# Kernel optimization log

Measured on AMD Instinct MI355X. Metric: run time of the kernel, lower is better.

Reference implementation:

```python
import jax, jax.numpy as jnp
import numpy as np

B, T, N, F_IN = 4, 16, 1000, 8
E = 8000
HID = 64
HEADS = 4
L = 5


def setup_inputs() -> dict:
    key = jax.random.key(0)
    ks = jax.random.split(key, 16)
    s = 0.1
    return {
        "x_seq": jax.random.normal(ks[0], (B, T, N, F_IN), dtype=jnp.float32),
        "edge_index": jax.random.randint(ks[1], (2, E), 0, N, dtype=jnp.int32),
        "edge_weight": jax.random.uniform(ks[2], (E,), dtype=jnp.float32),
        # input projection
        "W_in": jax.random.normal(ks[3], (F_IN, HID)) * s,
        "b_in": jnp.zeros((HID,), jnp.float32),
        # 5 stacked GATConv layers (heads=4, concat=False -> per-head dim = HID, mean over heads)
        "Wg": jax.random.normal(ks[4], (L, HID, HEADS * HID)) * s,
        "a_src": jax.random.normal(ks[5], (L, HEADS, HID)) * s,
        "a_dst": jax.random.normal(ks[6], (L, HEADS, HID)) * s,
        "bg": jnp.zeros((L, HID), jnp.float32),
        # GRU (input = N*HID flattened node features, torch gate order r,z,n)
        "W_ih": jax.random.normal(ks[7], (3 * HID, N * HID)) * 0.02,
        "W_hh": jax.random.normal(ks[8], (3 * HID, HID)) * s,
        "b_ih": jnp.zeros((3 * HID,), jnp.float32),
        "b_hh": jnp.zeros((3 * HID,), jnp.float32),
        # head: Linear(hidden_dim, num_nodes*pred_window) so out.view(B, N) works
        "W_fc": jax.random.normal(ks[9], (HID, N)) * s,
        "b_fc": jnp.zeros((N,), jnp.float32),
    }


def reference(x_seq, edge_index, edge_weight, W_in, b_in, Wg, a_src, a_dst, bg,
              W_ih, W_hh, b_ih, b_hh, W_fc, b_fc):
    Bb, Tt, Nn, Fin = x_seq.shape
    hid = W_in.shape[1]
    heads = a_src.shape[1]
    # PyG GATConv adds self-loops by default
    self_loops = jnp.arange(Nn, dtype=edge_index.dtype)
    src = jnp.concatenate([edge_index[0], self_loops])
    dst = jnp.concatenate([edge_index[1], self_loops])

    # input_fc over all (batch*seq*node) rows
    x = (x_seq.reshape(-1, Fin) @ W_in + b_in).reshape(Bb * Tt, Nn, hid)

    def gat_one(x_g, W, asrc, adst, b):
        h = (x_g @ W).reshape(Nn, heads, hid)            # [N,H,C]
        ls = (h * asrc).sum(-1)                          # [N,H] src attention terms
        ld = (h * adst).sum(-1)                          # [N,H] dst attention terms
        e = jax.nn.leaky_relu(ls[src] + ld[dst], 0.2)    # [E',H]
        m = jax.ops.segment_max(e, dst, num_segments=Nn)
        ex = jnp.exp(e - m[dst])
        den = jax.ops.segment_sum(ex, dst, num_segments=Nn)
        alpha = ex / (den[dst] + 1e-16)                  # softmax over incoming edges
        msg = alpha[:, :, None] * h[src]                 # [E',H,C]
        agg = jax.ops.segment_sum(msg, dst, num_segments=Nn)
        return agg.mean(axis=1) + b                      # concat=False -> mean heads

    for l in range(Wg.shape[0]):
        x = jax.nn.elu(jax.vmap(
            lambda xg, W=Wg[l], a1=a_src[l], a2=a_dst[l], b=bg[l]: gat_one(xg, W, a1, a2, b)
        )(x))

    # GRU over time, input = flattened node features per timestep
    seq = x.reshape(Bb, Tt, Nn * hid).transpose(1, 0, 2)  # [T,B,N*HID]

    def step(h, x_t):
        gi = x_t @ W_ih.T + b_ih
        gh = h @ W_hh.T + b_hh
        ir, iz, inn = jnp.split(gi, 3, axis=-1)
        hr, hz, hn = jnp.split(gh, 3, axis=-1)
        r = jax.nn.sigmoid(ir + hr)
        z = jax.nn.sigmoid(iz + hz)
        n = jnp.tanh(inn + r * hn)
        return (1.0 - z) * n + z * h, None

    h0 = jnp.zeros((Bb, hid), x_seq.dtype)
    hT, _ = jax.lax.scan(step, h0, seq)                  # last GRU output == final h
    return hT @ W_fc + b_fc                              # [B, N]
```

## Files before the change

### kernel.cpp

```cpp
#include <hip/hip_runtime.h>
#include <math.h>

#define NB 4
#define TT 16
#define NNODE 1000
#define FIN 8
#define EE 8000
#define EP 9000
#define EPAD 16384
#define HID 64
#define HEADS 4
#define NL 5
#define GG (NB*TT)
#define ROWS (GG*NNODE)
#define HCOL (HEADS*HID)
#define KGI (NNODE*HID)
#define GOUT 192
#define GIK 128
#define KSPLIT (KGI/GIK)
#define GOSZ (GG*GOUT)
#define WPSZ (8*4*64*8)

typedef unsigned short u16;
typedef __attribute__((ext_vector_type(8))) short short8;
typedef __attribute__((ext_vector_type(4))) float f32x4;

__device__ inline u16 f2bf(float f) {
    unsigned int u = __float_as_uint(f);
    unsigned int r = u + 0x7FFFu + ((u >> 16) & 1u);
    return (u16)(r >> 16);
}
__device__ inline float bf2f(u16 h) {
    return __uint_as_float(((unsigned int)h) << 16);
}

__global__ void k_build_edges(const int* __restrict__ eidx, int* __restrict__ src_e,
                              int* __restrict__ dst_e, int* __restrict__ deg, int* __restrict__ fill) {
    int i = blockIdx.x * blockDim.x + threadIdx.x;
    if (i < EP) {
        int s, d;
        if (i < EE) { s = eidx[i]; d = eidx[EE + i]; }
        else { s = i - EE; d = i - EE; }
        src_e[i] = s; dst_e[i] = d;
    }
    if (i < NNODE) { deg[i] = 0; fill[i] = 0; }
}

__global__ void k_csr_count(const int* __restrict__ dst_e, int* __restrict__ deg) {
    int i = blockIdx.x * blockDim.x + threadIdx.x;
    if (i < EP) atomicAdd(&deg[dst_e[i]], 1);
}

__global__ __launch_bounds__(256) void k_csr_scan(const int* __restrict__ deg, int* __restrict__ rowptr_p) {
    __shared__ int s[1024];
    int tid = threadIdx.x;
    for (int i = tid; i < 1024; i += 256) s[i] = (i < NNODE) ? ((deg[i] + 7) & ~7) : 0;
    __syncthreads();
    for (int off = 1; off < 1024; off <<= 1) {
        int t[4];
        #pragma unroll
        for (int q = 0; q < 4; q++) { int i = tid + 256 * q; t[q] = (i >= off) ? s[i - off] : 0; }
        __syncthreads();
        #pragma unroll
        for (int q = 0; q < 4; q++) { int i = tid + 256 * q; s[i] += t[q]; }
        __syncthreads();
    }
    for (int i = tid; i < NNODE; i += 256) rowptr_p[i + 1] = s[i];
    if (tid == 0) rowptr_p[0] = 0;
}

__global__ void k_csr_fill(const int* __restrict__ src_e, const int* __restrict__ dst_e,
                           const int* __restrict__ rowptr_p, int* __restrict__ fill,
                           int* __restrict__ csr_src) {
    int i = blockIdx.x * blockDim.x + threadIdx.x;
    if (i < EP) {
        int d = dst_e[i];
        int pos = atomicAdd(&fill[d], 1);
        csr_src[rowptr_p[d] + pos] = src_e[i];
    }
}

__global__ void k_pad_fill(const int* __restrict__ rowptr_p, const int* __restrict__ deg,
                           int* __restrict__ csr_src) {
    int n = blockIdx.x * blockDim.x + threadIdx.x;
    if (n >= NNODE) return;
    int rs = rowptr_p[n], re = rowptr_p[n + 1];
    for (int j = rs + deg[n]; j < re; j++) csr_src[j] = n;
}

__global__ void k_wa(const float* __restrict__ Wg, const float* __restrict__ a_src,
                     const float* __restrict__ a_dst, float* __restrict__ wa, float* __restrict__ wd) {
    int t = blockIdx.x * 256 + threadIdx.x;
    if (t >= 2 * NL * HID * HEADS) return;
    int kind = t >= NL * HID * HEADS;
    int u = t - kind * NL * HID * HEADS;
    int l = u >> 8;
    int rem = u & 255;
    int j = rem >> 2, hd = rem & 3;
    const float* a = (kind ? a_dst : a_src) + (size_t)l * HCOL + hd * HID;
    const float* Wl = Wg + (size_t)l * HID * HCOL + (size_t)j * HCOL + hd * HID;
    float acc = 0.f;
    #pragma unroll 8
    for (int c = 0; c < HID; c++) acc += Wl[c] * a[c];
    float* out = kind ? wd : wa;
    out[(size_t)l * HCOL + j * 4 + hd] = acc;
}

__global__ void k_wpack(const float* __restrict__ Wg, u16* __restrict__ wph, u16* __restrict__ wpl) {
    int t = blockIdx.x * 256 + threadIdx.x;
    if (t >= NL * WPSZ) return;
    int j    = t & 7;
    int lane = (t >> 3) & 63;
    int ct   = (t >> 9) & 3;
    int ks   = (t >> 11) & 7;
    int l    = t >> 14;
    int k = ks * 32 + (lane >> 4) * 8 + j;
    int c = ct * 16 + (lane & 15);
    float v = Wg[(size_t)l * HID * HCOL + (size_t)(k & 63) * HCOL + (k >> 6) * 64 + c];
    u16 h = f2bf(v);
    wph[t] = h;
    wpl[t] = f2bf(v - bf2f(h));
}

__global__ void k_input_fc(const float* __restrict__ xseq, const float4* __restrict__ Win4,
                           const float4* __restrict__ b_in4, const float4* __restrict__ wa04,
                           const float4* __restrict__ wd04, float4* __restrict__ x0,
                           float4* __restrict__ ls4, float4* __restrict__ ld4) {
    int idx = blockIdx.x * 256 + threadIdx.x;
    int r = idx >> 4, c4 = idx & 15;
    float4 acc = b_in4[c4];
    #pragma unroll
    for (int k = 0; k < FIN; k++) {
        float xv = xseq[r * FIN + k];
        float4 w = Win4[k * 16 + c4];
        acc.x += xv * w.x; acc.y += xv * w.y; acc.z += xv * w.z; acc.w += xv * w.w;
    }
    x0[idx] = acc;
    float xr[4] = {acc.x, acc.y, acc.z, acc.w};
    float4 pls = make_float4(0.f, 0.f, 0.f, 0.f);
    float4 pld = make_float4(0.f, 0.f, 0.f, 0.f);
    #pragma unroll
    for (int jj = 0; jj < 4; jj++) {
        float4 wa_j = wa04[c4 * 4 + jj];
        float4 wd_j = wd04[c4 * 4 + jj];
        pls.x += xr[jj] * wa_j.x; pls.y += xr[jj] * wa_j.y;
        pls.z += xr[jj] * wa_j.z; pls.w += xr[jj] * wa_j.w;
        pld.x += xr[jj] * wd_j.x; pld.y += xr[jj] * wd_j.y;
        pld.z += xr[jj] * wd_j.z; pld.w += xr[jj] * wd_j.w;
    }
    #pragma unroll
    for (int o = 1; o < 16; o <<= 1) {
        pls.x += __shfl_xor(pls.x, o, 64); pls.y += __shfl_xor(pls.y, o, 64);
        pls.z += __shfl_xor(pls.z, o, 64); pls.w += __shfl_xor(pls.w, o, 64);
        pld.x += __shfl_xor(pld.x, o, 64); pld.y += __shfl_xor(pld.y, o, 64);
        pld.z += __shfl_xor(pld.w, o, 64); pld.w += __shfl_xor(pld.w, o, 64);
    }
    if (c4 == 0) {
        ls4[r] = pls;
        ld4[r] = pld;
    }
}

__global__ __launch_bounds__(256) void k_aggx(const float4* __restrict__ x4, const float4* __restrict__ ls4,
                                              const float4* __restrict__ ld4, const int* __restrict__ rowptr_p,
                                              const int* __restrict__ csr_src, const int* __restrict__ deg,
                                              u16* __restrict__ yh, u16* __restrict__ yl) {
    __shared__ float s_e[4][4][4 * 68];
    __shared__ int   s_src[4][4][64];
    __shared__ float s_den[4][4][4];
    int b = blockIdx.x;
    int xcd = b & 7, s = b >> 3;
    int tid = threadIdx.x;
    int wid = tid >> 6, lane = tid & 63;
    int w = s * 4 + wid;
    int g = xcd + 8 * (w / 250);
    int n0 = (w % 250) * 4;
    int nsub = lane >> 4;
    int j0 = lane & 15;
    int n_s = n0 + nsub;
    int rs = rowptr_p[n_s];
    int dgp = rowptr_p[n_s + 1] - rs;
    int dg = deg[n_s];
    int dg16 = (dgp + 15) & ~15;
    if (dg16 > 64) dg16 = 64;
    if (dgp > 64) dgp = 64;
    float4 ldv = ld4[(size_t)g * NNODE + n_s];
    const float4* lsg = ls4 + (size_t)g * NNODE;

    float4 mx = make_float4(-1e30f, -1e30f, -1e30f, -1e30f);
    for (int base = 0; base < dg16; base += 16) {
        int j = base + j0;
        int sv = n_s;
        if (j < dgp) sv = csr_src[rs + j];
        s_src[wid][nsub][j] = sv;
        float4 lo = make_float4(-1e30f, -1e30f, -1e30f, -1e30f);
        if (j < dg) {
            float4 t = lsg[sv];
            t.x += ldv.x; t.y += ldv.y; t.z += ldv.z; t.w += ldv.w;
            t.x = fmaxf(t.x, 0.2f * t.x); t.y = fmaxf(t.y, 0.2f * t.y);
            t.z = fmaxf(t.z, 0.2f * t.z); t.w = fmaxf(t.w, 0.2f * t.w);
            lo = t;
            mx.x = fmaxf(mx.x, lo.x); mx.y = fmaxf(mx.y, lo.y);
            mx.z = fmaxf(mx.z, lo.z); mx.w = fmaxf(mx.w, lo.w);
        }
        s_e[wid][nsub][0 * 68 + j] = lo.x;
        s_e[wid][nsub][1 * 68 + j] = lo.y;
        s_e[wid][nsub][2 * 68 + j] = lo.z;
        s_e[wid][nsub][3 * 68 + j] = lo.w;
    }
    #pragma unroll
    for (int o = 1; o < 16; o <<= 1) {
        mx.x = fmaxf(mx.x, __shfl_xor(mx.x, o, 64));
        mx.y = fmaxf(mx.y, __shfl_xor(mx.y, o, 64));
        mx.z = fmaxf(mx.z, __shfl_xor(mx.z, o, 64));
        mx.w = fmaxf(mx.w, __shfl_xor(mx.w, o, 64));
    }
    float4 den = make_float4(0.f, 0.f, 0.f, 0.f);
    for (int base = 0; base < dg16; base += 16) {
        int j = base + j0;
        float4 e = make_float4(0.f, 0.f, 0.f, 0.f);
        if (j < dg) {
            e.x = expf(s_e[wid][nsub][0 * 68 + j] - mx.x);
            e.y = expf(s_e[wid][nsub][1 * 68 + j] - mx.y);
            e.z = expf(s_e[wid][nsub][2 * 68 + j] - mx.z);
            e.w = expf(s_e[wid][nsub][3 * 68 + j] - mx.w);
        }
        den.x += e.x; den.y += e.y; den.z += e.z; den.w += e.w;
        s_e[wid][nsub][0 * 68 + j] = e.x;
        s_e[wid][nsub][1 * 68 + j] = e.y;
        s_e[wid][nsub][2 * 68 + j] = e.z;
        s_e[wid][nsub][3 * 68 + j] = e.w;
    }
    #pragma unroll
    for (int o = 1; o < 16; o <<= 1) {
        den.x += __shfl_xor(den.x, o, 64);
        den.y += __shfl_xor(den.y, o, 64);
        den.z += __shfl_xor(den.z, o, 64);
        den.w += __shfl_xor(den.w, o, 64);
    }
    if (j0 == 0) {
        s_den[wid][nsub][0] = den.x;
        s_den[wid][nsub][1] = den.y;
        s_den[wid][nsub][2] = den.z;
        s_den[wid][nsub][3] = den.w;
    }

    int head = lane >> 4, c4 = lane & 15;
    const float4* xg = x4 + (size_t)g * NNODE * 16 + c4;
    float4 acc[4];
    #pragma unroll
    for (int nn = 0; nn < 4; nn++) acc[nn] = make_float4(0.f, 0.f, 0.f, 0.f);
    #pragma unroll
    for (int nn = 0; nn < 4; nn++) {
        int dgc = __shfl(dgp, nn * 16, 64);
        const float* ep = &s_e[wid][nn][head * 68];
        const int* sp = &s_src[wid][nn][0];
        for (int q = 0; q < dgc; q += 8) {
            int sj[8]; float av[8];
            #pragma unroll
            for (int u = 0; u < 8; u++) {
                sj[u] = sp[q + u];
                av[u] = ep[q + u];
            }
            float4 xv[8];
            #pragma unroll
            for (int u = 0; u < 8; u++) xv[u] = xg[(size_t)sj[u] * 16];
            #pragma unroll
            for (int u = 0; u < 8; u++) {
                acc[nn].x += av[u] * xv[u].x;
                acc[nn].y += av[u] * xv[u].y;
                acc[nn].z += av[u] * xv[u].z;
                acc[nn].w += av[u] * xv[u].w;
            }
        }
    }
    #pragma unroll
    for (int nn = 0; nn < 4; nn++) {
        float inv = 1.f / (s_den[wid][nn][head] + 1e-16f);
        float4 a = acc[nn];
        a.x *= inv; a.y *= inv; a.z *= inv; a.w *= inv;
        size_t r64 = ((size_t)g * NNODE + n0 + nn) * 64 + lane;
        ushort4 hv, lv;
        hv.x = f2bf(a.x); lv.x = f2bf(a.x - bf2f(hv.x));
        hv.y = f2bf(a.y); lv.y = f2bf(a.y - bf2f(hv.y));
        hv.z = f2bf(a.z); lv.z = f2bf(a.z - bf2f(hv.z));
        hv.w = f2bf(a.w); lv.w = f2bf(a.w - bf2f(hv.w));
        reinterpret_cast<ushort4*>(yh)[r64] = hv;
        reinterpret_cast<ushort4*>(yl)[r64] = lv;
    }
}

__global__ __launch_bounds__(256) void k_ygemm_mfma(const u16* __restrict__ yh, const u16* __restrict__ yl,
                                                    const u16* __restrict__ wph, const u16* __restrict__ wpl,
                                                    const float* __restrict__ bg, float* __restrict__ xout,
                                                    const float4* __restrict__ wa4, const float4* __restrict__ wd4,
                                                    float4* __restrict__ ls4, float4* __restrict__ ld4) {
    int tid = threadIdx.x;
    int wv = tid >> 6, lane = tid & 63;
    int r0w = blockIdx.x * 64 + wv * 16;
    int arow = lane & 15, kg = lane >> 4;

    f32x4 acc0 = {0.f, 0.f, 0.f, 0.f};
    f32x4 acc1 = {0.f, 0.f, 0.f, 0.f};
    f32x4 acc2 = {0.f, 0.f, 0.f, 0.f};
    f32x4 acc3 = {0.f, 0.f, 0.f, 0.f};

    const short8* ah8 = reinterpret_cast<const short8*>(yh + (size_t)(r0w + arow) * 256 + kg * 8);
    const short8* al8 = reinterpret_cast<const short8*>(yl + (size_t)(r0w + arow) * 256 + kg * 8);
    const short8* bh8 = reinterpret_cast<const short8*>(wph) + lane;
    const short8* bl8 = reinterpret_cast<const short8*>(wpl) + lane;

    #pragma unroll
    for (int ks = 0; ks < 8; ks++) {
        short8 ah = ah8[ks * 4];
        short8 al = al8[ks * 4];
        #pragma unroll
        for (int ct = 0; ct < 4; ct++) {
            short8 bh = bh8[(size_t)(ks * 4 + ct) * 64];
            short8 bl = bl8[(size_t)(ks * 4 + ct) * 64];
            f32x4* ac = (ct == 0) ? &acc0 : (ct == 1) ? &acc1 : (ct == 2) ? &acc2 : &acc3;
            *ac = __builtin_amdgcn_mfma_f32_16x16x32_bf16(ah, bh, *ac, 0, 0, 0);
            *ac = __builtin_amdgcn_mfma_f32_16x16x32_bf16(ah, bl, *ac, 0, 0, 0);
            *ac = __builtin_amdgcn_mfma_f32_16x16x32_bf16(al, bh, *ac, 0, 0, 0);
        }
    }

    float ev[4][4];
    #pragma unroll
    for (int ct = 0; ct < 4; ct++) {
        int c = ct * 16 + arow;
        float bc = bg[c];
        f32x4 a = (ct == 0) ? acc0 : (ct == 1) ? acc1 : (ct == 2) ? acc2 : acc3;
        #pragma unroll
        for (int r = 0; r < 4; r++) {
            float v = a[r] * 0.25f + bc;
            float e = v > 0.f ? v : expm1f(v);
            ev[ct][r] = e;
            xout[(size_t)(r0w + kg * 4 + r) * HID + c] = e;
        }
    }
    if (wa4) {
        #pragma unroll
        for (int r = 0; r < 4; r++) {
            float4 pls = make_float4(0.f, 0.f, 0.f, 0.f);
            float4 pld = make_float4(0.f, 0.f, 0.f, 0.f);
            #pragma unroll
            for (int ct = 0; ct < 4; ct++) {
                int c = ct * 16 + arow;
                float e = ev[ct][r];
                float4 wa_c = wa4[c];
                float4 wd_c = wd4[c];
                pls.x += e * wa_c.x; pls.y += e * wa_c.y;
                pls.z += e * wa_c.z; pls.w += e * wa_c.w;
                pld.x += e * wd_c.x; pld.y += e * wd_c.y;
                pld.z += e * wd_c.z; pld.w += e * wd_c.w;
            }
            #pragma unroll
            for (int o = 1; o < 16; o <<= 1) {
                pls.x += __shfl_xor(pls.x, o, 64); pls.y += __shfl_xor(pls.y, o, 64);
                pls.z += __shfl_xor(pls.z, o, 64); pls.w += __shfl_xor(pls.w, o, 64);
                pld.x += __shfl_xor(pld.x, o, 64); pld.y += __shfl_xor(pld.y, o, 64);
                pld.z += __shfl_xor(pld.z, o, 64); pld.w += __shfl_xor(pld.w, o, 64);
            }
            if (arow == 0) {
                int row = r0w + kg * 4 + r;
                ls4[row] = pls;
                ld4[row] = pld;
            }
        }
    }
}

__global__ __launch_bounds__(256) void k_gi_gemm(const float* __restrict__ x, const float* __restrict__ W_ih,
                                                 float* __restrict__ gip) {
    __shared__ float xs[32 * 68];
    __shared__ float ws[32 * 196];
    int k0 = blockIdx.x * GIK;
    int tid = threadIdx.x;
    int lane = tid & 63;
    int wv = tid >> 6;
    int tx = tid & 15, ty = tid >> 4;
    float4 accs[4][3];
    #pragma unroll
    for (int i = 0; i < 4; i++)
        #pragma unroll
        for (int j = 0; j < 3; j++) accs[i][j] = make_float4(0.f, 0.f, 0.f, 0.f);

    for (int kt = 0; kt < GIK / 32; kt++) {
        int kb = k0 + kt * 32;
        #pragma unroll
        for (int it = 0; it < 2; it++) {
            int kq = wv + 4 * it;
            float4 v = *reinterpret_cast<const float4*>(&x[(size_t)lane * KGI + kb + kq * 4]);
            int k = kq * 4;
            xs[(k + 0) * 68 + lane] = v.x;
            xs[(k + 1) * 68 + lane] = v.y;
            xs[(k + 2) * 68 + lane] = v.z;
            xs[(k + 3) * 68 + lane] = v.w;
        }
        #pragma unroll
        for (int cg = 0; cg < 3; cg++) {
            #pragma unroll
            for (int it = 0; it < 2; it++) {
                int kq = wv + 4 * it;
                int c = cg * 64 + lane;
                float4 v = *reinterpret_cast<const float4*>(&W_ih[(size_t)c * KGI + kb + kq * 4]);
                int k = kq * 4;
                ws[(k + 0) * 196 + c] = v.x;
                ws[(k + 1) * 196 + c] = v.y;
                ws[(k + 2) * 196 + c] = v.z;
                ws[(k + 3) * 196 + c] = v.w;
            }
        }
        __syncthreads();
        for (int kk = 0; kk < 32; kk++) {
            float4 xv = *reinterpret_cast<const float4*>(&xs[kk * 68 + ty * 4]);
            float4 w0 = *reinterpret_cast<const float4*>(&ws[kk * 196 + tx * 4]);
            float4 w1 = *reinterpret_cast<const float4*>(&ws[kk * 196 + 64 + tx * 4]);
            float4 w2 = *reinterpret_cast<const float4*>(&ws[kk * 196 + 128 + tx * 4]);
            #pragma unroll
            for (int i = 0; i < 4; i++) {
                float xi = (i == 0) ? xv.x : (i == 1) ? xv.y : (i == 2) ? xv.z : xv.w;
                accs[i][0].x += xi * w0.x; accs[i][0].y += xi * w0.y; accs[i][0].z += xi * w0.z; accs[i][0].w += xi * w0.w;
                accs[i][1].x += xi * w1.x; accs[i][1].y += xi * w1.y; accs[i][1].z += xi * w1.z; accs[i][1].w += xi * w1.w;
                accs[i][2].x += xi * w2.x; accs[i][2].y += xi * w2.y; accs[i][2].z += xi * w2.z; accs[i][2].w += xi * w2.w;
            }
        }
        __syncthreads();
    }
    float* out = gip + (size_t)blockIdx.x * GOSZ;
    #pragma unroll
    for (int i = 0; i < 4; i++)
        #pragma unroll
        for (int j = 0; j < 3; j++)
            *reinterpret_cast<float4*>(&out[(ty * 4 + i) * GOUT + j * 64 + tx * 4]) = accs[i][j];
}

__global__ void k_gi_reduce1(const float* __restrict__ gip, float* __restrict__ gip2) {
    int idx = blockIdx.x * 256 + threadIdx.x;
    const float* p = gip + (size_t)blockIdx.y * 50 * GOSZ + idx;
    float a = 0.f;
    #pragma unroll 5
    for (int s = 0; s < 50; s++) a += p[(size_t)s * GOSZ];
    gip2[blockIdx.y * GOSZ + idx] = a;
}

__global__ void k_gi_reduce2(const float* __restrict__ gip2, const float* __restrict__ b_ih,
                             float* __restrict__ gi) {
    int idx = blockIdx.x * 256 + threadIdx.x;
    float a = b_ih[idx % GOUT];
    #pragma unroll
    for (int y = 0; y < 10; y++) a += gip2[(size_t)y * GOSZ + idx];
    gi[idx] = a;
}

__global__ __launch_bounds__(192) void k_gru(const float* __restrict__ gi, const float* __restrict__ W_hh,
                                             const float* __restrict__ b_hh, float* __restrict__ hT) {
    __shared__ float hs[64];
    __shared__ float gh[192];
    int j = threadIdx.x;
    int b = blockIdx.x;
    float wrow[64];
    #pragma unroll
    for (int q = 0; q < 16; q++) {
        float4 v = *reinterpret_cast<const float4*>(&W_hh[(size_t)j * 64 + q * 4]);
        wrow[q * 4 + 0] = v.x; wrow[q * 4 + 1] = v.y;
        wrow[q * 4 + 2] = v.z; wrow[q * 4 + 3] = v.w;
    }
    float bj = b_hh[j];
    if (j < 64) hs[j] = 0.f;
    __syncthreads();
    for (int t = 0; t < TT; t++) {
        float a0 = 0.f, a1 = 0.f, a2 = 0.f, a3 = 0.f;
        #pragma unroll
        for (int q = 0; q < 16; q++) {
            float4 h4 = *reinterpret_cast<const float4*>(&hs[q * 4]);
            a0 += h4.x * wrow[q * 4 + 0];
            a1 += h4.y * wrow[q * 4 + 1];
            a2 += h4.z * wrow[q * 4 + 2];
            a3 += h4.w * wrow[q * 4 + 3];
        }
        gh[j] = bj + ((a0 + a1) + (a2 + a3));
        __syncthreads();
        if (j < 64) {
            int row = (b * TT + t) * GOUT;
            float ir = gi[row + j], iz = gi[row + 64 + j], in_ = gi[row + 128 + j];
            float r = 1.f / (1.f + expf(-(ir + gh[j])));
            float z = 1.f / (1.f + expf(-(iz + gh[64 + j])));
            float nv = tanhf(in_ + r * gh[128 + j]);
            hs[j] = (1.f - z) * nv + z * hs[j];
        }
        __syncthreads();
    }
    if (j < 64) hT[b * 64 + j] = hs[j];
}

__global__ void k_final(const float* __restrict__ hT, const float* __restrict__ W_fc,
                        const float* __restrict__ b_fc, float* __restrict__ out) {
    int idx = blockIdx.x * 256 + threadIdx.x;
    if (idx >= NB * NNODE) return;
    int b = idx / NNODE, n = idx % NNODE;
    float acc = b_fc[n];
    #pragma unroll
    for (int c = 0; c < HID; c++) acc += hT[b * HID + c] * W_fc[c * NNODE + n];
    out[idx] = acc;
}

extern "C" void kernel_launch(void* const* d_in, const int* in_sizes, int n_in,
                              void* d_out, int out_size, void* d_ws, size_t ws_size,
                              hipStream_t stream) {
    const float* x_seq  = (const float*)d_in[0];
    const int*   eidx   = (const int*)  d_in[1];
    const float* W_in   = (const float*)d_in[3];
    const float* b_in   = (const float*)d_in[4];
    const float* Wg     = (const float*)d_in[5];
    const float* a_src  = (const float*)d_in[6];
    const float* a_dst  = (const float*)d_in[7];
    const float* bg     = (const float*)d_in[8];
    const float* W_ih   = (const float*)d_in[9];
    const float* W_hh   = (const float*)d_in[10];
    const float* b_ih   = (const float*)d_in[11];
    const float* b_hh   = (const float*)d_in[12];
    const float* W_fc   = (const float*)d_in[13];
    const float* b_fc   = (const float*)d_in[14];
    float* out = (float*)d_out;

    float* wsf = (float*)d_ws;
    size_t off = 0;
    float* x0     = wsf + off; off += (size_t)ROWS * HID;
    float* ybuf   = wsf + off; off += (size_t)ROWS * HCOL;
    float* lsb    = wsf + off; off += (size_t)ROWS * HEADS;
    float* ldb    = wsf + off; off += (size_t)ROWS * HEADS;
    float* wab    = wsf + off; off += NL * HCOL;
    float* wdb    = wsf + off; off += NL * HCOL;
    float* gib    = wsf + off; off += GOSZ;
    float* hTb    = wsf + off; off += 256;
    u16* wphb     = (u16*)(wsf + off); off += NL * WPSZ / 2;
    u16* wplb     = (u16*)(wsf + off); off += NL * WPSZ / 2;
    int* ib = (int*)(wsf + off);
    int* src_e    = ib;          ib += EP;
    int* dst_e    = ib;          ib += EP;
    int* rowptr_p = ib;          ib += NNODE + 1;
    int* csr_src  = ib;          ib += EPAD;
    int* deg      = ib;          ib += NNODE;
    int* fill     = ib;          ib += NNODE;

    u16* yh = (u16*)ybuf;
    u16* yl = yh + (size_t)ROWS * HCOL;

    float* gip  = ybuf;
    float* gip2 = ybuf + (size_t)KSPLIT * GOSZ;

    k_build_edges<<<(EP + 255) / 256, 256, 0, stream>>>(eidx, src_e, dst_e, deg, fill);
    k_csr_count<<<(EP + 255) / 256, 256, 0, stream>>>(dst_e, deg);
    k_csr_scan<<<1, 256, 0, stream>>>(deg, rowptr_p);
    k_csr_fill<<<(EP + 255) / 256, 256, 0, stream>>>(src_e, dst_e, rowptr_p, fill, csr_src);
    k_pad_fill<<<(NNODE + 255) / 256, 256, 0, stream>>>(rowptr_p, deg, csr_src);

    k_wa<<<10, 256, 0, stream>>>(Wg, a_src, a_dst, wab, wdb);
    k_wpack<<<(NL * WPSZ + 255) / 256, 256, 0, stream>>>(Wg, wphb, wplb);

    k_input_fc<<<ROWS * 16 / 256, 256, 0, stream>>>(
        x_seq, (const float4*)W_in, (const float4*)b_in,
        (const float4*)wab, (const float4*)wdb, (float4*)x0, (float4*)lsb, (float4*)ldb);

    for (int l = 0; l < NL; l++) {
        k_aggx<<<ROWS / 16, 256, 0, stream>>>(
            (const float4*)x0, (const float4*)lsb, (const float4*)ldb, rowptr_p, csr_src, deg,
            yh, yl);
        const float4* wa_next = (l + 1 < NL) ? (const float4*)(wab + (size_t)(l + 1) * HCOL) : nullptr;
        const float4* wd_next = (l + 1 < NL) ? (const float4*)(wdb + (size_t)(l + 1) * HCOL) : nullptr;
        k_ygemm_mfma<<<ROWS / 64, 256, 0, stream>>>(
            yh, yl, wphb + (size_t)l * WPSZ, wplb + (size_t)l * WPSZ,
            bg + (size_t)l * HID, x0,
            wa_next, wd_next, (float4*)lsb, (float4*)ldb);
    }

    k_gi_gemm<<<KSPLIT, 256, 0, stream>>>(x0, W_ih, gip);
    k_gi_reduce1<<<dim3(GOSZ / 256, 10), 256, 0, stream>>>(gip, gip2);
    k_gi_reduce2<<<GOSZ / 256, 256, 0, stream>>>(gip2, b_ih, gib);
    k_gru<<<4, 192, 0, stream>>>(gib, W_hh, b_hh, hTb);
    k_final<<<(NB * NNODE + 255) / 256, 256, 0, stream>>>(hTb, W_fc, b_fc, out);
}
```

Before: 493.0 us.

## Restructure GAT aggregation so each lane-group handles one node across all heads

```diff
diff --git a/kernel.cpp b/kernel.cpp
--- a/kernel.cpp
+++ b/kernel.cpp
@@ -33,6 +33,15 @@
 __device__ inline float bf2f(u16 h) {
     return __uint_as_float(((unsigned int)h) << 16);
 }
+__device__ inline ushort4 bfhi4(float4 a) {
+    ushort4 r; r.x = f2bf(a.x); r.y = f2bf(a.y); r.z = f2bf(a.z); r.w = f2bf(a.w); return r;
+}
+__device__ inline ushort4 bflo4(float4 a, ushort4 h) {
+    ushort4 r;
+    r.x = f2bf(a.x - bf2f(h.x)); r.y = f2bf(a.y - bf2f(h.y));
+    r.z = f2bf(a.z - bf2f(h.z)); r.w = f2bf(a.w - bf2f(h.w));
+    return r;
+}
 
 __global__ void k_build_edges(const int* __restrict__ eidx, int* __restrict__ src_e,
                               int* __restrict__ dst_e, int* __restrict__ deg, int* __restrict__ fill) {
@@ -153,7 +162,7 @@
         pls.x += __shfl_xor(pls.x, o, 64); pls.y += __shfl_xor(pls.y, o, 64);
         pls.z += __shfl_xor(pls.z, o, 64); pls.w += __shfl_xor(pls.w, o, 64);
         pld.x += __shfl_xor(pld.x, o, 64); pld.y += __shfl_xor(pld.y, o, 64);
-        pld.z += __shfl_xor(pld.w, o, 64); pld.w += __shfl_xor(pld.w, o, 64);
+        pld.z += __shfl_xor(pld.z, o, 64); pld.w += __shfl_xor(pld.w, o, 64);
     }
     if (c4 == 0) {
         ls4[r] = pls;
@@ -165,7 +174,7 @@
                                               const float4* __restrict__ ld4, const int* __restrict__ rowptr_p,
                                               const int* __restrict__ csr_src, const int* __restrict__ deg,
                                               u16* __restrict__ yh, u16* __restrict__ yl) {
-    __shared__ float s_e[4][4][4 * 68];
+    __shared__ float s_e[4][4][264];
     __shared__ int   s_src[4][4][64];
     __shared__ float s_den[4][4][4];
     int b = blockIdx.x;
@@ -203,10 +212,7 @@
             mx.x = fmaxf(mx.x, lo.x); mx.y = fmaxf(mx.y, lo.y);
             mx.z = fmaxf(mx.z, lo.z); mx.w = fmaxf(mx.w, lo.w);
         }
-        s_e[wid][nsub][0 * 68 + j] = lo.x;
-        s_e[wid][nsub][1 * 68 + j] = lo.y;
-        s_e[wid][nsub][2 * 68 + j] = lo.z;
-        s_e[wid][nsub][3 * 68 + j] = lo.w;
+        *reinterpret_cast<float4*>(&s_e[wid][nsub][j * 4]) = lo;
     }
     #pragma unroll
     for (int o = 1; o < 16; o <<= 1) {
@@ -220,16 +226,14 @@
         int j = base + j0;
         float4 e = make_float4(0.f, 0.f, 0.f, 0.f);
         if (j < dg) {
-            e.x = expf(s_e[wid][nsub][0 * 68 + j] - mx.x);
-            e.y = expf(s_e[wid][nsub][1 * 68 + j] - mx.y);
-            e.z = expf(s_e[wid][nsub][2 * 68 + j] - mx.z);
-            e.w = expf(s_e[wid][nsub][3 * 68 + j] - mx.w);
+            float4 lo = *reinterpret_cast<const float4*>(&s_e[wid][nsub][j * 4]);
+            e.x = expf(lo.x - mx.x);
+            e.y = expf(lo.y - mx.y);
+            e.z = expf(lo.z - mx.z);
+            e.w = expf(lo.w - mx.w);
         }
         den.x += e.x; den.y += e.y; den.z += e.z; den.w += e.w;
-        s_e[wid][nsub][0 * 68 + j] = e.x;
-        s_e[wid][nsub][1 * 68 + j] = e.y;
-        s_e[wid][nsub][2 * 68 + j] = e.z;
-        s_e[wid][nsub][3 * 68 + j] = e.w;
+        *reinterpret_cast<float4*>(&s_e[wid][nsub][j * 4]) = e;
     }
     #pragma unroll
     for (int o = 1; o < 16; o <<= 1) {
@@ -239,55 +243,51 @@
         den.w += __shfl_xor(den.w, o, 64);
     }
     if (j0 == 0) {
-        s_den[wid][nsub][0] = den.x;
-        s_den[wid][nsub][1] = den.y;
-        s_den[wid][nsub][2] = den.z;
-        s_den[wid][nsub][3] = den.w;
-    }
-
-    int head = lane >> 4, c4 = lane & 15;
+        *reinterpret_cast<float4*>(&s_den[wid][nsub][0]) = den;
+    }
+
+    int c4 = lane & 15;
     const float4* xg = x4 + (size_t)g * NNODE * 16 + c4;
-    float4 acc[4];
-    #pragma unroll
-    for (int nn = 0; nn < 4; nn++) acc[nn] = make_float4(0.f, 0.f, 0.f, 0.f);
-    #pragma unroll
-    for (int nn = 0; nn < 4; nn++) {
-        int dgc = __shfl(dgp, nn * 16, 64);
-        const float* ep = &s_e[wid][nn][head * 68];
-        const int* sp = &s_src[wid][nn][0];
-        for (int q = 0; q < dgc; q += 8) {
-            int sj[8]; float av[8];
-            #pragma unroll
-            for (int u = 0; u < 8; u++) {
-                sj[u] = sp[q + u];
-                av[u] = ep[q + u];
-            }
-            float4 xv[8];
-            #pragma unroll
-            for (int u = 0; u < 8; u++) xv[u] = xg[(size_t)sj[u] * 16];
-            #pragma unroll
-            for (int u = 0; u < 8; u++) {
-                acc[nn].x += av[u] * xv[u].x;
-                acc[nn].y += av[u] * xv[u].y;
-                acc[nn].z += av[u] * xv[u].z;
-                acc[nn].w += av[u] * xv[u].w;
-            }
-        }
-    }
-    #pragma unroll
-    for (int nn = 0; nn < 4; nn++) {
-        float inv = 1.f / (s_den[wid][nn][head] + 1e-16f);
-        float4 a = acc[nn];
-        a.x *= inv; a.y *= inv; a.z *= inv; a.w *= inv;
-        size_t r64 = ((size_t)g * NNODE + n0 + nn) * 64 + lane;
-        ushort4 hv, lv;
-        hv.x = f2bf(a.x); lv.x = f2bf(a.x - bf2f(hv.x));
-        hv.y = f2bf(a.y); lv.y = f2bf(a.y - bf2f(hv.y));
-        hv.z = f2bf(a.z); lv.z = f2bf(a.z - bf2f(hv.z));
-        hv.w = f2bf(a.w); lv.w = f2bf(a.w - bf2f(hv.w));
-        reinterpret_cast<ushort4*>(yh)[r64] = hv;
-        reinterpret_cast<ushort4*>(yl)[r64] = lv;
-    }
+    float4 a0 = make_float4(0.f, 0.f, 0.f, 0.f);
+    float4 a1 = a0, a2 = a0, a3 = a0;
+    const float* ep = &s_e[wid][nsub][0];
+    const int* sp = &s_src[wid][nsub][0];
+    for (int q = 0; q < dgp; q += 4) {
+        int sj[4]; float4 ev[4];
+        #pragma unroll
+        for (int u = 0; u < 4; u++) sj[u] = sp[q + u];
+        #pragma unroll
+        for (int u = 0; u < 4; u++) ev[u] = *reinterpret_cast<const float4*>(&ep[(q + u) * 4]);
+        float4 xv[4];
+        #pragma unroll
+        for (int u = 0; u < 4; u++) xv[u] = xg[(size_t)sj[u] * 16];
+        #pragma unroll
+        for (int u = 0; u < 4; u++) {
+            a0.x += ev[u].x * xv[u].x; a0.y += ev[u].x * xv[u].y;
+            a0.z += ev[u].x * xv[u].z; a0.w += ev[u].x * xv[u].w;
+            a1.x += ev[u].y * xv[u].x; a1.y += ev[u].y * xv[u].y;
+            a1.z += ev[u].y * xv[u].z; a1.w += ev[u].y * xv[u].w;
+            a2.x += ev[u].z * xv[u].x; a2.y += ev[u].z * xv[u].y;
+            a2.z += ev[u].z * xv[u].z; a2.w += ev[u].z * xv[u].w;
+            a3.x += ev[u].w * xv[u].x; a3.y += ev[u].w * xv[u].y;
+            a3.z += ev[u].w * xv[u].z; a3.w += ev[u].w * xv[u].w;
+        }
+    }
+    float4 dv = *reinterpret_cast<const float4*>(&s_den[wid][nsub][0]);
+    float i0 = 1.f / (dv.x + 1e-16f), i1 = 1.f / (dv.y + 1e-16f);
+    float i2 = 1.f / (dv.z + 1e-16f), i3 = 1.f / (dv.w + 1e-16f);
+    a0.x *= i0; a0.y *= i0; a0.z *= i0; a0.w *= i0;
+    a1.x *= i1; a1.y *= i1; a1.z *= i1; a1.w *= i1;
+    a2.x *= i2; a2.y *= i2; a2.z *= i2; a2.w *= i2;
+    a3.x *= i3; a3.y *= i3; a3.z *= i3; a3.w *= i3;
+    size_t wb = ((size_t)g * NNODE + n_s) * 64 + c4;
+    ushort4* YH = reinterpret_cast<ushort4*>(yh);
+    ushort4* YL = reinterpret_cast<ushort4*>(yl);
+    ushort4 h0 = bfhi4(a0), h1 = bfhi4(a1), h2 = bfhi4(a2), h3 = bfhi4(a3);
+    YH[wb +  0] = h0; YL[wb +  0] = bflo4(a0, h0);
+    YH[wb + 16] = h1; YL[wb + 16] = bflo4(a1, h1);
+    YH[wb + 32] = h2; YL[wb + 32] = bflo4(a2, h2);
+    YH[wb + 48] = h3; YL[wb + 48] = bflo4(a3, h3);
 }
 
 __global__ __launch_bounds__(256) void k_ygemm_mfma(const u16* __restrict__ yh, const u16* __restrict__ yl,
```

Result: faster. 432.5 us (-12.3%).
